# Kernel optimization log

Measured on AMD Instinct MI355X. Metric: run time of the kernel, lower is better.

## Reference

```python
import jax, jax.numpy as jnp
import numpy as np

N_NODES = 100000
N_EDGES = 1600000
IN_FEAT = 64
OUT_FEAT = 64
K_ORDER = 1
BN_EPS = 1e-5


def setup_inputs() -> dict:
    key = jax.random.key(0)
    ks = jax.random.split(key, 8)
    feature = jax.random.normal(ks[0], (N_NODES, IN_FEAT), dtype=jnp.float32)
    sp_embeddings = jax.random.normal(ks[1], (N_NODES, 16), dtype=jnp.float32)
    edge_src = jax.random.randint(ks[2], (N_EDGES,), 0, N_NODES, dtype=jnp.int32)
    edge_dst = jax.random.randint(ks[3], (N_EDGES,), 0, N_NODES, dtype=jnp.int32)
    edge_order = jax.random.randint(ks[4], (N_EDGES,), 0, K_ORDER + 1, dtype=jnp.int32)
    # xavier_normal over (in, out) fan dims
    std = float(np.sqrt(2.0 / (IN_FEAT + OUT_FEAT)))
    linear = jax.random.normal(ks[5], (K_ORDER + 1, IN_FEAT, OUT_FEAT), dtype=jnp.float32) * std
    mlp_w = jax.random.normal(ks[6], (OUT_FEAT, OUT_FEAT), dtype=jnp.float32) * std
    mlp_b = jnp.zeros((OUT_FEAT,), dtype=jnp.float32)
    bn_gamma = jnp.ones((OUT_FEAT,), dtype=jnp.float32)
    bn_beta = jnp.zeros((OUT_FEAT,), dtype=jnp.float32)
    return {
        "feature": feature,
        "sp_embeddings": sp_embeddings,
        "linear": linear,
        "mlp_w": mlp_w,
        "mlp_b": mlp_b,
        "bn_gamma": bn_gamma,
        "bn_beta": bn_beta,
        "edge_src": edge_src,
        "edge_dst": edge_dst,
        "edge_order": edge_order,
    }


def reference(feature, sp_embeddings, linear, mlp_w, mlp_b, bn_gamma, bn_beta,
              edge_src, edge_dst, edge_order):
    # msg_fun: gather per-edge weight matrix by edge order, batched matvec
    W_e = linear[edge_order]          # [E, in, out]
    h_src = feature[edge_src]          # [E, in]
    msg = jnp.einsum('eio,ei->eo', W_e, h_src)  # [E, out]
    # agg_fun: scatter-sum messages into destination nodes
    h = jax.ops.segment_sum(msg, edge_dst, num_segments=N_NODES)  # [N, out]
    # mlp: Linear -> ReLU -> BatchNorm1d (training mode: batch stats)
    h = jax.nn.relu(h @ mlp_w.T + mlp_b)
    mean = jnp.mean(h, axis=0)
    var = jnp.var(h, axis=0)  # biased, matching torch BN normalization
    h = (h - mean) * jax.lax.rsqrt(var + BN_EPS) * bn_gamma + bn_beta
    # shortcut=False -> no residual; sp_embeddings unused by forward
    return h
```

## Files before the change

### kernel.cpp

```cpp
#include <hip/hip_runtime.h>

#define N_NODES 100000
#define N_EDGES 1600000
#define NBUCK 1563
#define NBLK 128
#define PER_BLK 12500
#define MAX_BE 2048


__device__ __forceinline__ unsigned short f2bf(float x) {
  unsigned u = __float_as_uint(x);
  unsigned r = (u + 0x7FFFu + ((u >> 16) & 1u)) >> 16;
  return (unsigned short)r;
}

__global__ __launch_bounds__(256) void prep_U(const float* __restrict__ linear,
                                              const float* __restrict__ mlp_w,
                                              float* __restrict__ U) {
  int idx = blockIdx.x * 256 + threadIdx.x;
  int o = idx & 63;
  int ki = idx >> 6;
  int k = ki >> 6, i = ki & 63;
  float acc = 0.f;
#pragma unroll 8
  for (int j = 0; j < 64; ++j)
    acc += linear[ki * 64 + j] * mlp_w[o * 64 + j];
  U[i * 128 + k * 64 + o] = acc;
}

__global__ __launch_bounds__(256) void prep_B(const float* __restrict__ feature,
                                              const float* __restrict__ U,
                                              unsigned short* __restrict__ B) {
  __shared__ float Us[64 * 128];
  for (int i = threadIdx.x; i < 64 * 128; i += 256) Us[i] = U[i];
  __syncthreads();
  int row = blockIdx.x * 256 + threadIdx.x;
  if (row >= N_NODES) return;
  const float4* Fr = reinterpret_cast<const float4*>(feature + (size_t)row * 64);
#pragma unroll
  for (int k = 0; k < 2; ++k) {
    float acc[64];
#pragma unroll
    for (int o = 0; o < 64; ++o) acc[o] = 0.f;
#pragma unroll 4
    for (int i4 = 0; i4 < 16; ++i4) {
      float4 a = Fr[i4];
      float av[4] = {a.x, a.y, a.z, a.w};
#pragma unroll
      for (int u = 0; u < 4; ++u) {
        const float* Ur = &Us[(i4 * 4 + u) * 128 + k * 64];
#pragma unroll
        for (int o = 0; o < 64; ++o) acc[o] = fmaf(av[u], Ur[o], acc[o]);
      }
    }
    ushort4* Bp = reinterpret_cast<ushort4*>(B + (((size_t)row * 2 + k) << 6));
#pragma unroll
    for (int o4 = 0; o4 < 16; ++o4) {
      ushort4 pk;
      pk.x = f2bf(acc[o4 * 4 + 0]);
      pk.y = f2bf(acc[o4 * 4 + 1]);
      pk.z = f2bf(acc[o4 * 4 + 2]);
      pk.w = f2bf(acc[o4 * 4 + 3]);
      Bp[o4] = pk;
    }
  }
}

__global__ __launch_bounds__(256) void countA(const int* __restrict__ edst,
                                              unsigned* __restrict__ cntg) {
  __shared__ unsigned h[NBUCK];
  for (int i = threadIdx.x; i < NBUCK; i += 256) h[i] = 0;
  __syncthreads();
  const int k = blockIdx.x;
  const int beg = k * PER_BLK, end = beg + PER_BLK;
  for (int e = beg + (int)threadIdx.x; e < end; e += 256)
    atomicAdd(&h[((unsigned)edst[e]) >> 6], 1u);
  __syncthreads();
  for (int i = threadIdx.x; i < NBUCK; i += 256)
    cntg[(size_t)k * NBUCK + i] = h[i];
}

__global__ __launch_bounds__(256) void scanT1(unsigned* __restrict__ cntg,
                                              unsigned* __restrict__ tot) {
  const int lane = threadIdx.x & 63;
  const int wv = threadIdx.x >> 6;
  const int b = blockIdx.x * 4 + wv;
  if (b >= NBUCK) return;
  unsigned c0 = cntg[(size_t)lane * NBUCK + b];
  unsigned c1 = cntg[(size_t)(64 + lane) * NBUCK + b];
  unsigned i0 = c0, i1 = c1;
#pragma unroll
  for (int d = 1; d < 64; d <<= 1) {
    unsigned n0 = __shfl_up(i0, d);
    unsigned n1 = __shfl_up(i1, d);
    if (lane >= d) { i0 += n0; i1 += n1; }
  }
  unsigned tot0 = __shfl(i0, 63);
  unsigned tot1 = __shfl(i1, 63);
  cntg[(size_t)lane * NBUCK + b] = i0 - c0;
  cntg[(size_t)(64 + lane) * NBUCK + b] = tot0 + i1 - c1;
  if (lane == 0) tot[b] = tot0 + tot1;
}

__global__ __launch_bounds__(256) void scanT2(const unsigned* __restrict__ tot,
                                              unsigned* __restrict__ base) {
  __shared__ unsigned sh[256];
  const int t = threadIdx.x;
  unsigned local[7];
  unsigned s = 0;
#pragma unroll
  for (int i = 0; i < 7; ++i) {
    int idx = t * 7 + i;
    local[i] = (idx < NBUCK) ? tot[idx] : 0u;
    s += local[i];
  }
  sh[t] = s;
  __syncthreads();
#pragma unroll
  for (int off = 1; off < 256; off <<= 1) {
    unsigned v = (t >= off) ? sh[t - off] : 0u;
    __syncthreads();
    sh[t] += v;
    __syncthreads();
  }
  unsigned run = sh[t] - s;
#pragma unroll
  for (int i = 0; i < 7; ++i) {
    int idx = t * 7 + i;
    if (idx < NBUCK) { base[idx] = run; run += local[i]; }
  }
  if (t == 0) base[NBUCK] = N_EDGES;
}

__global__ __launch_bounds__(256) void fillB(const int* __restrict__ esrc,
                                             const int* __restrict__ edst,
                                             const int* __restrict__ eord,
                                             const unsigned* __restrict__ cntg,
                                             const unsigned* __restrict__ base,
                                             unsigned* __restrict__ pay) {
  __shared__ unsigned curL[NBUCK];
  const int k = blockIdx.x;
  for (int i = threadIdx.x; i < NBUCK; i += 256)
    curL[i] = base[i] + cntg[(size_t)k * NBUCK + i];
  __syncthreads();
  const int beg = k * PER_BLK, end = beg + PER_BLK;
  for (int e = beg + (int)threadIdx.x; e < end; e += 256) {
    unsigned d = (unsigned)edst[e];
    unsigned pos = atomicAdd(&curL[d >> 6], 1u);
    pay[pos] = ((d & 63u) << 18) | ((unsigned)esrc[e] << 1) | (unsigned)eord[e];
  }
}

__global__ __launch_bounds__(256) void bgather(const unsigned* __restrict__ base,
                                               const unsigned* __restrict__ pay,
                                               const unsigned short* __restrict__ B,
                                               const float* __restrict__ bias,
                                               float* __restrict__ out,
                                               double* __restrict__ stats) {
  __shared__ unsigned hist[64];
  __shared__ unsigned offsL[65];
  __shared__ unsigned curN[64];
  __shared__ unsigned pay_s[MAX_BE];
  __shared__ double dd0[4][64];
  __shared__ double dd1[4][64];
  const int tid = threadIdx.x;
  const int lane = tid & 63;
  const int wv = tid >> 6;
  const int b = blockIdx.x;
  const unsigned base0 = base[b];
  const unsigned n_e = base[b + 1] - base0;

  if (tid < 64) hist[tid] = 0;
  __syncthreads();
  for (unsigned i = tid; i < n_e; i += 256)
    atomicAdd(&hist[pay[base0 + i] >> 18], 1u);
  __syncthreads();
  if (wv == 0) {
    unsigned hv = hist[lane];
    unsigned inc = hv;
#pragma unroll
    for (int d = 1; d < 64; d <<= 1) {
      unsigned n = __shfl_up(inc, d);
      if (lane >= d) inc += n;
    }
    offsL[lane + 1] = inc;
    if (lane == 0) offsL[0] = 0;
    curN[lane] = inc - hv;
  }
  __syncthreads();
  for (unsigned i = tid; i < n_e; i += 256) {
    unsigned w = pay[base0 + i];
    unsigned pos = atomicAdd(&curN[w >> 18], 1u);
    pay_s[pos] = w;
  }
  __syncthreads();

  const int g = tid >> 4;
  const int sl = tid & 15;
  const int c0 = sl << 2;
  const float4 bo4 = *reinterpret_cast<const float4*>(bias + c0);
  double s0[4] = {0, 0, 0, 0}, s1[4] = {0, 0, 0, 0};

#pragma unroll
  for (int i = 0; i < 4; ++i) {
    const int nl = (g << 2) + i;
    const int ng = (b << 6) + nl;
    unsigned e = offsL[nl];
    const unsigned e1 = offsL[nl + 1];
    float s[4] = {0.f, 0.f, 0.f, 0.f};
    while (e < e1) {
      unsigned rem = e1 - e;
      int cnt = rem < 8u ? (int)rem : 8;
      unsigned p[8];
      uint2 v[8];
#pragma unroll
      for (int j = 0; j < 8; ++j)
        p[j] = pay_s[e + (j < cnt ? (unsigned)j : 0u)];
#pragma unroll
      for (int j = 0; j < 8; ++j)
        v[j] = *reinterpret_cast<const uint2*>(
            B + (((size_t)(p[j] & 0x3FFFFu)) << 6) + c0);
#pragma unroll
      for (int j = 0; j < 8; ++j) {
        if (j < cnt) {
          s[0] += __uint_as_float(v[j].x << 16);
          s[1] += __uint_as_float(v[j].x & 0xFFFF0000u);
          s[2] += __uint_as_float(v[j].y << 16);
          s[3] += __uint_as_float(v[j].y & 0xFFFF0000u);
        }
      }
      e += cnt;
    }
    if (ng < N_NODES) {
      float4 r;
      r.x = fmaxf(s[0] + bo4.x, 0.f);
      r.y = fmaxf(s[1] + bo4.y, 0.f);
      r.z = fmaxf(s[2] + bo4.z, 0.f);
      r.w = fmaxf(s[3] + bo4.w, 0.f);
      *reinterpret_cast<float4*>(out + ((size_t)ng << 6) + c0) = r;
      s0[0] += (double)r.x; s1[0] += (double)r.x * (double)r.x;
      s0[1] += (double)r.y; s1[1] += (double)r.y * (double)r.y;
      s0[2] += (double)r.z; s1[2] += (double)r.z * (double)r.z;
      s0[3] += (double)r.w; s1[3] += (double)r.w * (double)r.w;
    }
  }

#pragma unroll
  for (int q = 0; q < 4; ++q) {
    double v0 = s0[q], v1 = s1[q];
    v0 += __shfl_xor(v0, 16); v0 += __shfl_xor(v0, 32);
    v1 += __shfl_xor(v1, 16); v1 += __shfl_xor(v1, 32);
    s0[q] = v0; s1[q] = v1;
  }
  if ((lane & 48) == 0) {
#pragma unroll
    for (int q = 0; q < 4; ++q) {
      dd0[wv][c0 + q] = s0[q];
      dd1[wv][c0 + q] = s1[q];
    }
  }
  __syncthreads();
  if (tid < 64) {
    double t0 = dd0[0][tid] + dd0[1][tid] + dd0[2][tid] + dd0[3][tid];
    double t1 = dd1[0][tid] + dd1[1][tid] + dd1[2][tid] + dd1[3][tid];
    atomicAdd(&stats[tid], t0);
    atomicAdd(&stats[64 + tid], t1);
  }
}

__global__ __launch_bounds__(256) void bn_apply(float* __restrict__ h,
                                                const double* __restrict__ stats,
                                                const float* __restrict__ gamma,
                                                const float* __restrict__ beta) {
  const int lane = threadIdx.x & 63;
  double mean = stats[lane] * (1.0 / N_NODES);
  double var = stats[64 + lane] * (1.0 / N_NODES) - mean * mean;
  float inv = (float)(1.0 / sqrt(var + 1e-5));
  float scale = gamma[lane] * inv;
  float shift = beta[lane] - (float)mean * scale;
  int wid = (blockIdx.x * 256 + threadIdx.x) >> 6;
  const int nw = gridDim.x * 4;
  for (int r = wid; r < N_NODES; r += nw) {
    size_t idx = ((size_t)r << 6) + lane;
    h[idx] = h[idx] * scale + shift;
  }
}

extern "C" void kernel_launch(void* const* d_in, const int* in_sizes, int n_in,
                              void* d_out, int out_size, void* d_ws, size_t ws_size,
                              hipStream_t stream) {
  const float* feature = (const float*)d_in[0];
  const float* linear = (const float*)d_in[2];
  const float* mlp_w  = (const float*)d_in[3];
  const float* mlp_b  = (const float*)d_in[4];
  const float* gamma  = (const float*)d_in[5];
  const float* beta   = (const float*)d_in[6];
  const int* esrc = (const int*)d_in[7];
  const int* edst = (const int*)d_in[8];
  const int* eord = (const int*)d_in[9];
  float* out = (float*)d_out;

  char* basep = (char*)d_ws;
  unsigned*       cntg  = (unsigned*)(basep);
  unsigned*       tot   = (unsigned*)(basep + 800256);
  unsigned*       base  = (unsigned*)(basep + 806512);
  double*         stats = (double*)  (basep + 812800);
  float*          U     = (float*)   (basep + 813824);
  unsigned*       pay   = (unsigned*)(basep + 846592);
  unsigned short* B     = (unsigned short*)(basep + 7246592);

  hipMemsetAsync(stats, 0, 1024, stream);
  prep_U<<<32, 256, 0, stream>>>(linear, mlp_w, U);
  countA<<<NBLK, 256, 0, stream>>>(edst, cntg);
  scanT1<<<(NBUCK + 3) / 4, 256, 0, stream>>>(cntg, tot);
  scanT2<<<1, 256, 0, stream>>>(tot, base);
  fillB<<<NBLK, 256, 0, stream>>>(esrc, edst, eord, cntg, base, pay);
  prep_B<<<(N_NODES + 255) / 256, 256, 0, stream>>>(feature, U, B);
  bgather<<<NBUCK, 256, 0, stream>>>(base, pay, B, mlp_b, out, stats);
  bn_apply<<<1024, 256, 0, stream>>>(out, stats, gamma, beta);
}
```

Before: 178.9 us.

## Double bucketing blocks, widen count/fill threads, compute two rows per thread in prep_B

The edge bucketing now runs on 256 blocks of 512 threads, each handling 6250 edges, instead of 128 blocks of 256 threads. The transposed scan is rewritten so each lane sums four block counts before the wave scan. prep_B now computes two feature rows per thread, reusing each shared-memory U load for two FMAs. This roughly doubles the accumulator registers, which may lower occupancy or cause spills. The workspace offsets are moved to fit the larger count table.

```diff
diff --git a/kernel.cpp b/kernel.cpp
--- a/kernel.cpp
+++ b/kernel.cpp
@@ -3,8 +3,8 @@
 #define N_NODES 100000
 #define N_EDGES 1600000
 #define NBUCK 1563
-#define NBLK 128
-#define PER_BLK 12500
+#define NBLK 256
+#define PER_BLK 6250
 #define MAX_BE 2048
 
 
@@ -34,49 +34,71 @@
   __shared__ float Us[64 * 128];
   for (int i = threadIdx.x; i < 64 * 128; i += 256) Us[i] = U[i];
   __syncthreads();
-  int row = blockIdx.x * 256 + threadIdx.x;
-  if (row >= N_NODES) return;
-  const float4* Fr = reinterpret_cast<const float4*>(feature + (size_t)row * 64);
+  const int ra = blockIdx.x * 512 + threadIdx.x;
+  const int rb = ra + 256;
+  const bool va = ra < N_NODES, vb = rb < N_NODES;
+  const float4* Fa = reinterpret_cast<const float4*>(feature + (size_t)(va ? ra : 0) * 64);
+  const float4* Fb = reinterpret_cast<const float4*>(feature + (size_t)(vb ? rb : 0) * 64);
 #pragma unroll
   for (int k = 0; k < 2; ++k) {
-    float acc[64];
-#pragma unroll
-    for (int o = 0; o < 64; ++o) acc[o] = 0.f;
-#pragma unroll 4
+    float acc0[64], acc1[64];
+#pragma unroll
+    for (int o = 0; o < 64; ++o) { acc0[o] = 0.f; acc1[o] = 0.f; }
+#pragma unroll 2
     for (int i4 = 0; i4 < 16; ++i4) {
-      float4 a = Fr[i4];
+      float4 a = Fa[i4];
+      float4 cc = Fb[i4];
       float av[4] = {a.x, a.y, a.z, a.w};
+      float cv[4] = {cc.x, cc.y, cc.z, cc.w};
 #pragma unroll
       for (int u = 0; u < 4; ++u) {
         const float* Ur = &Us[(i4 * 4 + u) * 128 + k * 64];
 #pragma unroll
-        for (int o = 0; o < 64; ++o) acc[o] = fmaf(av[u], Ur[o], acc[o]);
+        for (int o = 0; o < 64; ++o) {
+          float w = Ur[o];
+          acc0[o] = fmaf(av[u], w, acc0[o]);
+          acc1[o] = fmaf(cv[u], w, acc1[o]);
+        }
       }
     }
-    ushort4* Bp = reinterpret_cast<ushort4*>(B + (((size_t)row * 2 + k) << 6));
-#pragma unroll
-    for (int o4 = 0; o4 < 16; ++o4) {
-      ushort4 pk;
-      pk.x = f2bf(acc[o4 * 4 + 0]);
-      pk.y = f2bf(acc[o4 * 4 + 1]);
-      pk.z = f2bf(acc[o4 * 4 + 2]);
-      pk.w = f2bf(acc[o4 * 4 + 3]);
-      Bp[o4] = pk;
-    }
-  }
-}
-
-__global__ __launch_bounds__(256) void countA(const int* __restrict__ edst,
+    if (va) {
+      ushort4* Bp = reinterpret_cast<ushort4*>(B + (((size_t)ra * 2 + k) << 6));
+#pragma unroll
+      for (int o4 = 0; o4 < 16; ++o4) {
+        ushort4 pk;
+        pk.x = f2bf(acc0[o4 * 4 + 0]);
+        pk.y = f2bf(acc0[o4 * 4 + 1]);
+        pk.z = f2bf(acc0[o4 * 4 + 2]);
+        pk.w = f2bf(acc0[o4 * 4 + 3]);
+        Bp[o4] = pk;
+      }
+    }
+    if (vb) {
+      ushort4* Bp = reinterpret_cast<ushort4*>(B + (((size_t)rb * 2 + k) << 6));
+#pragma unroll
+      for (int o4 = 0; o4 < 16; ++o4) {
+        ushort4 pk;
+        pk.x = f2bf(acc1[o4 * 4 + 0]);
+        pk.y = f2bf(acc1[o4 * 4 + 1]);
+        pk.z = f2bf(acc1[o4 * 4 + 2]);
+        pk.w = f2bf(acc1[o4 * 4 + 3]);
+        Bp[o4] = pk;
+      }
+    }
+  }
+}
+
+__global__ __launch_bounds__(512) void countA(const int* __restrict__ edst,
                                               unsigned* __restrict__ cntg) {
   __shared__ unsigned h[NBUCK];
-  for (int i = threadIdx.x; i < NBUCK; i += 256) h[i] = 0;
+  for (int i = threadIdx.x; i < NBUCK; i += 512) h[i] = 0;
   __syncthreads();
   const int k = blockIdx.x;
   const int beg = k * PER_BLK, end = beg + PER_BLK;
-  for (int e = beg + (int)threadIdx.x; e < end; e += 256)
+  for (int e = beg + (int)threadIdx.x; e < end; e += 512)
     atomicAdd(&h[((unsigned)edst[e]) >> 6], 1u);
   __syncthreads();
-  for (int i = threadIdx.x; i < NBUCK; i += 256)
+  for (int i = threadIdx.x; i < NBUCK; i += 512)
     cntg[(size_t)k * NBUCK + i] = h[i];
 }
 
@@ -86,20 +108,27 @@
   const int wv = threadIdx.x >> 6;
   const int b = blockIdx.x * 4 + wv;
   if (b >= NBUCK) return;
-  unsigned c0 = cntg[(size_t)lane * NBUCK + b];
-  unsigned c1 = cntg[(size_t)(64 + lane) * NBUCK + b];
-  unsigned i0 = c0, i1 = c1;
+  unsigned c[4];
+  unsigned lsum = 0;
+#pragma unroll
+  for (int j = 0; j < 4; ++j) {
+    c[j] = cntg[(size_t)(lane * 4 + j) * NBUCK + b];
+    lsum += c[j];
+  }
+  unsigned inc = lsum;
 #pragma unroll
   for (int d = 1; d < 64; d <<= 1) {
-    unsigned n0 = __shfl_up(i0, d);
-    unsigned n1 = __shfl_up(i1, d);
-    if (lane >= d) { i0 += n0; i1 += n1; }
-  }
-  unsigned tot0 = __shfl(i0, 63);
-  unsigned tot1 = __shfl(i1, 63);
-  cntg[(size_t)lane * NBUCK + b] = i0 - c0;
-  cntg[(size_t)(64 + lane) * NBUCK + b] = tot0 + i1 - c1;
-  if (lane == 0) tot[b] = tot0 + tot1;
+    unsigned n = __shfl_up(inc, d);
+    if (lane >= d) inc += n;
+  }
+  unsigned run = inc - lsum;
+#pragma unroll
+  for (int j = 0; j < 4; ++j) {
+    cntg[(size_t)(lane * 4 + j) * NBUCK + b] = run;
+    run += c[j];
+  }
+  unsigned total = __shfl(inc, 63);
+  if (lane == 0) tot[b] = total;
 }
 
 __global__ __launch_bounds__(256) void scanT2(const unsigned* __restrict__ tot,
@@ -132,7 +161,7 @@
   if (t == 0) base[NBUCK] = N_EDGES;
 }
 
-__global__ __launch_bounds__(256) void fillB(const int* __restrict__ esrc,
+__global__ __launch_bounds__(512) void fillB(const int* __restrict__ esrc,
                                              const int* __restrict__ edst,
                                              const int* __restrict__ eord,
                                              const unsigned* __restrict__ cntg,
@@ -140,11 +169,11 @@
                                              unsigned* __restrict__ pay) {
   __shared__ unsigned curL[NBUCK];
   const int k = blockIdx.x;
-  for (int i = threadIdx.x; i < NBUCK; i += 256)
+  for (int i = threadIdx.x; i < NBUCK; i += 512)
     curL[i] = base[i] + cntg[(size_t)k * NBUCK + i];
   __syncthreads();
   const int beg = k * PER_BLK, end = beg + PER_BLK;
-  for (int e = beg + (int)threadIdx.x; e < end; e += 256) {
+  for (int e = beg + (int)threadIdx.x; e < end; e += 512) {
     unsigned d = (unsigned)edst[e];
     unsigned pos = atomicAdd(&curL[d >> 6], 1u);
     pay[pos] = ((d & 63u) << 18) | ((unsigned)esrc[e] << 1) | (unsigned)eord[e];
@@ -302,20 +331,20 @@
 
   char* basep = (char*)d_ws;
   unsigned*       cntg  = (unsigned*)(basep);
-  unsigned*       tot   = (unsigned*)(basep + 800256);
-  unsigned*       base  = (unsigned*)(basep + 806512);
-  double*         stats = (double*)  (basep + 812800);
-  float*          U     = (float*)   (basep + 813824);
-  unsigned*       pay   = (unsigned*)(basep + 846592);
-  unsigned short* B     = (unsigned short*)(basep + 7246592);
-
-  hipMemsetAsync(stats, 0, 1024, stream);
+  unsigned*       tot   = (unsigned*)(basep + 1600512);
+  unsigned*       base  = (unsigned*)(basep + 1606768);
+  double*         stats = (double*)  (basep + 1613056);
+  float*          U     = (float*)   (basep + 1614080);
+  unsigned*       pay   = (unsigned*)(basep + 1646848);
+  unsigned short* B     = (unsigned short*)(basep + 8046848);
+
+  (void)hipMemsetAsync(stats, 0, 1024, stream);
   prep_U<<<32, 256, 0, stream>>>(linear, mlp_w, U);
-  countA<<<NBLK, 256, 0, stream>>>(edst, cntg);
+  countA<<<NBLK, 512, 0, stream>>>(edst, cntg);
   scanT1<<<(NBUCK + 3) / 4, 256, 0, stream>>>(cntg, tot);
   scanT2<<<1, 256, 0, stream>>>(tot, base);
-  fillB<<<NBLK, 256, 0, stream>>>(esrc, edst, eord, cntg, base, pay);
-  prep_B<<<(N_NODES + 255) / 256, 256, 0, stream>>>(feature, U, B);
+  fillB<<<NBLK, 512, 0, stream>>>(esrc, edst, eord, cntg, base, pay);
+  prep_B<<<(N_NODES + 511) / 512, 256, 0, stream>>>(feature, U, B);
   bgather<<<NBUCK, 256, 0, stream>>>(base, pay, B, mlp_b, out, stats);
   bn_apply<<<1024, 256, 0, stream>>>(out, stats, gamma, beta);
 }
```

Result: faster. 168.6 us (-5.8%).
